# Kernel optimization log

Measured on AMD Instinct MI355X. Metric: run time of the kernel, lower is better.

The kernel has to match this reference:

```python
import jax, jax.numpy as jnp
import numpy as np

EMBED_DIM = 768
NUM_HEADS = 12
HEAD_DIM = EMBED_DIM // NUM_HEADS
B, L = 1, 2048


def setup_inputs() -> dict:
    key = jax.random.key(0)
    ks = jax.random.split(key, 10)
    D = EMBED_DIM
    s = 1.0 / np.sqrt(D)
    x = jax.random.normal(ks[0], (B, L, D), dtype=jnp.float32)
    Wq = jax.random.uniform(ks[1], (D, D), jnp.float32, -s, s)
    bq = jax.random.uniform(ks[2], (D,), jnp.float32, -s, s)
    Wk = jax.random.uniform(ks[3], (D, D), jnp.float32, -s, s)
    bk = jax.random.uniform(ks[4], (D,), jnp.float32, -s, s)
    Wv = jax.random.uniform(ks[5], (D, D), jnp.float32, -s, s)
    bv = jax.random.uniform(ks[6], (D,), jnp.float32, -s, s)
    Wo = jax.random.uniform(ks[7], (D, D), jnp.float32, -s, s)
    bo = jax.random.uniform(ks[8], (D,), jnp.float32, -s, s)
    theta = jnp.zeros((1, NUM_HEADS, 1, 1), dtype=jnp.float32)
    return {"x": x, "Wq": Wq, "bq": bq, "Wk": Wk, "bk": bk,
            "Wv": Wv, "bv": bv, "Wo": Wo, "bo": bo, "theta": theta}


def _heads(t):
    # [B,L,D] -> [B,H,L,d_k]
    b, l, d = t.shape
    return t.reshape(b, l, NUM_HEADS, HEAD_DIM).transpose(0, 2, 1, 3)


def reference(x, Wq, bq, Wk, bk, Wv, bv, Wo, bo, theta):
    b, l, d = x.shape
    d_k = HEAD_DIM
    q = _heads(x @ Wq.T + bq)  # [B,H,L,dk]
    k = _heads(x @ Wk.T + bk)
    v = _heads(x @ Wv.T + bv)
    # squared pairwise L2 distance (== torch.cdist(q,k,p=2)**2), scaled by d_k
    qn = jnp.sum(q * q, axis=-1, keepdims=True)          # [B,H,L,1]
    kn = jnp.sum(k * k, axis=-1, keepdims=True)          # [B,H,L,1]
    qk = jnp.einsum('bhid,bhjd->bhij', q, k)             # [B,H,L,L]
    dist_sq = jnp.maximum(qn + kn.transpose(0, 1, 3, 2) - 2.0 * qk, 0.0) / d_k
    # global max over the full LxL matrix per (B,H)
    dist_max = jnp.max(dist_sq, axis=(-1, -2), keepdims=True)
    dist_norm = dist_sq / (dist_max + 1e-6)
    dsexp = jnp.exp(theta)                               # [1,H,1,1]
    attn_logits = jnp.exp(-dsexp * dist_norm)            # [B,H,L,L]
    attn_weights = jax.nn.softmax(attn_logits, axis=-1)
    context = jnp.einsum('bhij,bhjd->bhid', attn_weights, v)  # [B,H,L,dk]
    context = context.transpose(0, 2, 1, 3).reshape(b, l, d)
    output = context @ Wo.T + bo
    return output, attn_weights.mean(axis=1)
```

## Files before the change

### kernel.cpp

```cpp
#include <hip/hip_runtime.h>
#include <hip/hip_bf16.h>


typedef __bf16 bf16_t;
typedef bf16_t bf16x8 __attribute__((ext_vector_type(8)));
typedef float f32x4 __attribute__((ext_vector_type(4)));

#define L_SEQ 2048
#define DIM 768
#define NH 12
#define DKH 64
#define JSPLIT 4
#define LOG2E 1.44269504f

__device__ __forceinline__ f32x4 mfma16(bf16x8 a, bf16x8 b, f32x4 c_) {
  return __builtin_amdgcn_mfma_f32_16x16x32_bf16(a, b, c_, 0, 0, 0);
}


struct Tile2 { bf16x8 r[2]; };

__device__ __forceinline__ void tile_load(const bf16_t* __restrict__ src, int stride,
                                          Tile2& t_, int tid) {
#pragma unroll
  for (int c = 0; c < 2; ++c) {
    int chunk = tid + c * 256;
    t_.r[c] = *(const bf16x8*)&src[(size_t)(chunk >> 3) * stride + (chunk & 7) * 8];
  }
}

__device__ __forceinline__ void tile_write(bf16_t (*dst)[72], const Tile2& t_, int tid) {
#pragma unroll
  for (int c = 0; c < 2; ++c) {
    int chunk = tid + c * 256;
    *(bf16x8*)&dst[chunk >> 3][(chunk & 7) * 8] = t_.r[c];
  }
}

__device__ __forceinline__ void mfma_nt64(bf16_t (*As)[72], bf16_t (*Bs)[72],
                                          int wid, int lane, f32x4 acc[4]) {
#pragma unroll
  for (int ks = 0; ks < 2; ++ks) {
    bf16x8 a = *(const bf16x8*)&As[wid * 16 + (lane & 15)][ks * 32 + (lane >> 4) * 8];
#pragma unroll
    for (int nt = 0; nt < 4; ++nt) {
      bf16x8 b = *(const bf16x8*)&Bs[nt * 16 + (lane & 15)][ks * 32 + (lane >> 4) * 8];
      acc[nt] = mfma16(a, b, acc[nt]);
    }
  }
}


__global__ void cast_x(const float* __restrict__ in, bf16_t* __restrict__ out, int n4) {
  int i = blockIdx.x * 256 + threadIdx.x;
  if (i >= n4) return;
  float4 v = ((const float4*)in)[i];
  bf16_t* o = out + (size_t)i * 4;
  o[0] = (bf16_t)v.x; o[1] = (bf16_t)v.y; o[2] = (bf16_t)v.z; o[3] = (bf16_t)v.w;
}

__global__ void cast_w4(const float* __restrict__ w0, const float* __restrict__ w1,
                        const float* __restrict__ w2, const float* __restrict__ w3,
                        bf16_t* __restrict__ o0, bf16_t* __restrict__ o1,
                        bf16_t* __restrict__ o2, bf16_t* __restrict__ o3, int n4) {
  int i = blockIdx.x * 256 + threadIdx.x;
  if (i >= n4) return;
  const float* in = blockIdx.y == 0 ? w0 : blockIdx.y == 1 ? w1 : blockIdx.y == 2 ? w2 : w3;
  bf16_t* out = blockIdx.y == 0 ? o0 : blockIdx.y == 1 ? o1 : blockIdx.y == 2 ? o2 : o3;
  float4 v = ((const float4*)in)[i];
  bf16_t* o = out + (size_t)i * 4;
  o[0] = (bf16_t)v.x; o[1] = (bf16_t)v.y; o[2] = (bf16_t)v.z; o[3] = (bf16_t)v.w;
}


__global__ __launch_bounds__(256) void gemm_qkv(const bf16_t* __restrict__ x,
                                                const bf16_t* __restrict__ Bq,
                                                const bf16_t* __restrict__ Bk,
                                                const bf16_t* __restrict__ Bv,
                                                const float* __restrict__ bq,
                                                const float* __restrict__ bk,
                                                const float* __restrict__ bv,
                                                bf16_t* __restrict__ qo,
                                                bf16_t* __restrict__ ko,
                                                bf16_t* __restrict__ vto,
                                                float* __restrict__ qn,
                                                float* __restrict__ kn) {
  __shared__ bf16_t As[2][64][72];
  __shared__ bf16_t Bs[2][64][72];
  const int z = blockIdx.z;
  const bf16_t* B = z == 0 ? Bq : z == 1 ? Bk : Bv;
  const float* bias = z == 0 ? bq : z == 1 ? bk : bv;
  const int tid = threadIdx.x, wid = tid >> 6, lane = tid & 63;
  const int c = lane & 15, hi = lane >> 4;
  const int m0 = blockIdx.y * 64, n0 = blockIdx.x * 64;
  Tile2 at, bt;
  tile_load(x + (size_t)m0 * DIM, DIM, at, tid);
  tile_load(B + (size_t)n0 * DIM, DIM, bt, tid);
  f32x4 acc[4] = {};
  for (int kk = 0; kk < 12; ++kk) {
    tile_write(As[kk & 1], at, tid);
    tile_write(Bs[kk & 1], bt, tid);
    __syncthreads();
    if (kk < 11) {
      tile_load(x + (size_t)m0 * DIM + (kk + 1) * 64, DIM, at, tid);
      tile_load(B + (size_t)n0 * DIM + (kk + 1) * 64, DIM, bt, tid);
    }
    mfma_nt64(As[kk & 1], Bs[kk & 1], wid, lane, acc);
    __syncthreads();
  }
  const int r0 = wid * 16 + hi * 4;
  float ss[4] = {0.f, 0.f, 0.f, 0.f};
#pragma unroll
  for (int nt = 0; nt < 4; ++nt) {
    int cc = n0 + nt * 16 + c;
    float bv_ = bias[cc];
    int h = cc >> 6, d = cc & 63;
#pragma unroll
    for (int r = 0; r < 4; ++r) {
      int mm = m0 + r0 + r;
      float val = acc[nt][r] + bv_;
      if (z == 2) {
        vto[(size_t)cc * L_SEQ + mm] = (bf16_t)val;
      } else {
        bf16_t* out = z == 0 ? qo : ko;
        out[((size_t)h * L_SEQ + mm) * 64 + d] = (bf16_t)val;
        ss[r] = fmaf(val, val, ss[r]);
      }
    }
  }
  if (z < 2) {
#pragma unroll
    for (int s = 1; s < 16; s <<= 1)
#pragma unroll
      for (int r = 0; r < 4; ++r) ss[r] += __shfl_xor(ss[r], s);
    if (c == 0) {
      float* norm = z == 0 ? qn : kn;
      int h = n0 >> 6;
#pragma unroll
      for (int r = 0; r < 4; ++r) norm[h * L_SEQ + m0 + r0 + r] = ss[r];
    }
  }
}

__global__ __launch_bounds__(256) void gemm_out(const bf16_t* __restrict__ A,
                                                const bf16_t* __restrict__ B,
                                                const float* __restrict__ bias,
                                                float* __restrict__ out) {
  __shared__ bf16_t As[2][64][72];
  __shared__ bf16_t Bs[2][64][72];
  const int tid = threadIdx.x, wid = tid >> 6, lane = tid & 63;
  const int c = lane & 15, hi = lane >> 4;
  const int m0 = blockIdx.y * 64, n0 = blockIdx.x * 64;
  Tile2 at, bt;
  tile_load(A + (size_t)m0 * DIM, DIM, at, tid);
  tile_load(B + (size_t)n0 * DIM, DIM, bt, tid);
  f32x4 acc[4] = {};
  for (int kk = 0; kk < 12; ++kk) {
    tile_write(As[kk & 1], at, tid);
    tile_write(Bs[kk & 1], bt, tid);
    __syncthreads();
    if (kk < 11) {
      tile_load(A + (size_t)m0 * DIM + (kk + 1) * 64, DIM, at, tid);
      tile_load(B + (size_t)n0 * DIM + (kk + 1) * 64, DIM, bt, tid);
    }
    mfma_nt64(As[kk & 1], Bs[kk & 1], wid, lane, acc);
    __syncthreads();
  }
  const int r0 = wid * 16 + hi * 4;
#pragma unroll
  for (int nt = 0; nt < 4; ++nt) {
    int cc = n0 + nt * 16 + c;
    float bv = bias[cc];
#pragma unroll
    for (int r = 0; r < 4; ++r)
      out[(size_t)(m0 + r0 + r) * DIM + cc] = acc[nt][r] + bv;
  }
}


__global__ __launch_bounds__(256) void maxdist(const bf16_t* __restrict__ q,
                                               const bf16_t* __restrict__ k,
                                               const float* __restrict__ qn,
                                               const float* __restrict__ kn,
                                               float* __restrict__ blockmax) {
  __shared__ bf16_t Qs[64][72];
  __shared__ bf16_t Ks[64][72];
  __shared__ float wmax[4];
  const int it = blockIdx.x, jc = blockIdx.y, h = blockIdx.z;
  const int i0 = it * 64, jbase = jc * (L_SEQ / JSPLIT);
  const int tid = threadIdx.x, wid = tid >> 6, lane = tid & 63;
  const int c = lane & 15, hi = lane >> 4;
  Tile2 qt, kt;
  tile_load(q + ((size_t)h * L_SEQ + i0) * DKH, DKH, qt, tid);
  tile_write(Qs, qt, tid);
  tile_load(k + ((size_t)h * L_SEQ + jbase) * DKH, DKH, kt, tid);
  const int r0 = wid * 16 + hi * 4;
  float qnr[4];
#pragma unroll
  for (int r = 0; r < 4; ++r) qnr[r] = qn[h * L_SEQ + i0 + r0 + r];
  float m = 0.f;
  const int NT = L_SEQ / 64 / JSPLIT;
  for (int t = 0; t < NT; ++t) {
    tile_write(Ks, kt, tid);
    __syncthreads();
    if (t < NT - 1)
      tile_load(k + ((size_t)h * L_SEQ + jbase + (t + 1) * 64) * DKH, DKH, kt, tid);
    f32x4 acc[4] = {};
    mfma_nt64(Qs, Ks, wid, lane, acc);
#pragma unroll
    for (int nt = 0; nt < 4; ++nt) {
      float knc = kn[h * L_SEQ + jbase + t * 64 + nt * 16 + c];
#pragma unroll
      for (int r = 0; r < 4; ++r)
        m = fmaxf(m, fmaf(-2.f, acc[nt][r], qnr[r] + knc));
    }
    __syncthreads();
  }
#pragma unroll
  for (int s = 1; s < 64; s <<= 1) m = fmaxf(m, __shfl_xor(m, s));
  if (lane == 0) wmax[wid] = m;
  __syncthreads();
  if (tid == 0) {
    float bm = fmaxf(fmaxf(wmax[0], wmax[1]), fmaxf(wmax[2], wmax[3]));
    blockmax[(h * JSPLIT + jc) * (L_SEQ / 64) + it] = fmaxf(bm, 0.f) * (1.f / 64.f);
  }
}

__global__ void reduce_dmax(const float* __restrict__ blockmax, float* __restrict__ dmax) {
  __shared__ float wm[2];
  const int h = blockIdx.x, tid = threadIdx.x, lane = tid & 63, wid = tid >> 6;
  float m = blockmax[h * 128 + tid];
#pragma unroll
  for (int s = 1; s < 64; s <<= 1) m = fmaxf(m, __shfl_xor(m, s));
  if (lane == 0) wm[wid] = m;
  __syncthreads();
  if (tid == 0) dmax[h] = fmaxf(wm[0], wm[1]);
}

__global__ __launch_bounds__(256) void fusedctx_p(const bf16_t* __restrict__ q,
                                                  const bf16_t* __restrict__ k,
                                                  const bf16_t* __restrict__ vt,
                                                  const float* __restrict__ qn,
                                                  const float* __restrict__ kn,
                                                  const float* __restrict__ dmax,
                                                  const float* __restrict__ theta,
                                                  float* __restrict__ denP,
                                                  float* __restrict__ ctxP) {
  __shared__ bf16_t Qs[64][72];
  __shared__ bf16_t Ks[64][72];
  __shared__ bf16_t Vs[64][72];
  __shared__ bf16_t Ws[64][72];
  const int it = blockIdx.x, jc = blockIdx.y, h = blockIdx.z;
  const int i0 = it * 64, jbase = jc * (L_SEQ / 2);
  const int tid = threadIdx.x, wid = tid >> 6, lane = tid & 63;
  const int c = lane & 15, hi = lane >> 4;
  const float sc = __expf(theta[h]) * (1.f / 64.f) / (dmax[h] + 1e-6f);
  const float twosc = 2.f * sc;
  Tile2 qt, kt, vtr;
  tile_load(q + ((size_t)h * L_SEQ + i0) * DKH, DKH, qt, tid);
  tile_write(Qs, qt, tid);
  tile_load(k + ((size_t)h * L_SEQ + jbase) * DKH, DKH, kt, tid);
  tile_load(vt + (size_t)h * DKH * L_SEQ + jbase, L_SEQ, vtr, tid);
  const int r0 = wid * 16 + hi * 4;
  float aq[4];
#pragma unroll
  for (int r = 0; r < 4; ++r) aq[r] = sc * qn[h * L_SEQ + i0 + r0 + r];
  float psum[4] = {0.f, 0.f, 0.f, 0.f};
  f32x4 cacc[4] = {};
  const int NT = L_SEQ / 2 / 64;
  for (int t = 0; t < NT; ++t) {
    tile_write(Ks, kt, tid);
    tile_write(Vs, vtr, tid);
    __syncthreads();
    if (t < NT - 1) {
      tile_load(k + ((size_t)h * L_SEQ + jbase + (t + 1) * 64) * DKH, DKH, kt, tid);
      tile_load(vt + (size_t)h * DKH * L_SEQ + jbase + (t + 1) * 64, L_SEQ, vtr, tid);
    }
    f32x4 acc[4] = {};
    mfma_nt64(Qs, Ks, wid, lane, acc);
#pragma unroll
    for (int nt = 0; nt < 4; ++nt) {
      float bkn = -sc * kn[h * L_SEQ + jbase + t * 64 + nt * 16 + c];
#pragma unroll
      for (int r = 0; r < 4; ++r) {
        float tt = fminf(fmaf(twosc, acc[nt][r], bkn - aq[r]), 0.f);
        float w = __expf(__expf(tt));
        psum[r] += w;
        Ws[r0 + r][nt * 16 + c] = (bf16_t)w;
      }
    }
    __syncthreads();
    mfma_nt64(Vs, Ws, wid, lane, cacc);
    __syncthreads();
  }
#pragma unroll
  for (int s = 1; s < 16; s <<= 1)
#pragma unroll
    for (int r = 0; r < 4; ++r) psum[r] += __shfl_xor(psum[r], s);
  if (c == 0)
#pragma unroll
    for (int r = 0; r < 4; ++r)
      denP[(size_t)(h * 2 + jc) * L_SEQ + i0 + r0 + r] = psum[r];
  float* P = ctxP + ((size_t)(h * 2 + jc) * 32 + it) * 4096;
#pragma unroll
  for (int nt = 0; nt < 4; ++nt)
    *(f32x4*)&P[(nt * 16 + c) * 64 + r0] = cacc[nt];
}

__global__ __launch_bounds__(256) void ctx_combine(const float* __restrict__ denP,
                                                   const float* __restrict__ ctxP,
                                                   float* __restrict__ den,
                                                   bf16_t* __restrict__ ctx) {
  __shared__ float invL[64];
  const int it = blockIdx.x, h = blockIdx.y, tid = threadIdx.x;
  const int i0 = it * 64;
  if (tid < 64) {
    float d0 = denP[(size_t)(h * 2) * L_SEQ + i0 + tid] +
               denP[(size_t)(h * 2 + 1) * L_SEQ + i0 + tid];
    den[h * L_SEQ + i0 + tid] = d0;
    invL[tid] = 1.f / d0;
  }
  __syncthreads();
  const float* P0 = ctxP + ((size_t)(h * 2) * 32 + it) * 4096;
  const float* P1 = ctxP + ((size_t)(h * 2 + 1) * 32 + it) * 4096;
  const int il = tid >> 2, db = (tid & 3) * 16;
  const float inv = invL[il];
  bf16_t* dst = ctx + (size_t)(i0 + il) * DIM + h * 64 + db;
#pragma unroll
  for (int half = 0; half < 2; ++half) {
    bf16x8 o;
#pragma unroll
    for (int e = 0; e < 2; ++e) {
      f32x4 v0 = *(const f32x4*)&P0[il * 64 + db + half * 8 + e * 4];
      f32x4 v1 = *(const f32x4*)&P1[il * 64 + db + half * 8 + e * 4];
#pragma unroll
      for (int j = 0; j < 4; ++j) o[e * 4 + j] = (bf16_t)((v0[j] + v1[j]) * inv);
    }
    *(bf16x8*)&dst[half * 8] = o;
  }
}

__global__ __launch_bounds__(256) void attnmean(const bf16_t* __restrict__ q,
                                                const bf16_t* __restrict__ k,
                                                const float* __restrict__ qn,
                                                const float* __restrict__ kn,
                                                const float* __restrict__ dmax,
                                                const float* __restrict__ theta,
                                                const float* __restrict__ den,
                                                float* __restrict__ out1) {
  __shared__ bf16_t Qs[2][64][72];
  __shared__ bf16_t Ks[2][64][72];
  const int i0 = blockIdx.y * 64, j0 = blockIdx.x * 64;
  const int tid = threadIdx.x, wid = tid >> 6, lane = tid & 63;
  const int c = lane & 15, hi = lane >> 4;
  const int r0 = wid * 16 + hi * 4;
  Tile2 qt, kt;
  tile_load(q + (size_t)i0 * DKH, DKH, qt, tid);
  tile_load(k + (size_t)j0 * DKH, DKH, kt, tid);
  float macc[4][4] = {};
  for (int h = 0; h < NH; ++h) {
    tile_write(Qs[h & 1], qt, tid);
    tile_write(Ks[h & 1], kt, tid);
    __syncthreads();
    if (h < NH - 1) {
      tile_load(q + ((size_t)(h + 1) * L_SEQ + i0) * DKH, DKH, qt, tid);
      tile_load(k + ((size_t)(h + 1) * L_SEQ + j0) * DKH, DKH, kt, tid);
    }
    const float sc = __expf(theta[h]) * (1.f / 64.f) / (dmax[h] + 1e-6f);
    const float twosc = 2.f * sc;
    f32x4 acc[4] = {};
    mfma_nt64(Qs[h & 1], Ks[h & 1], wid, lane, acc);
    float aq[4], invl[4];
#pragma unroll
    for (int r = 0; r < 4; ++r) {
      aq[r] = sc * qn[h * L_SEQ + i0 + r0 + r];
      invl[r] = 1.f / den[h * L_SEQ + i0 + r0 + r];
    }
#pragma unroll
    for (int nt = 0; nt < 4; ++nt) {
      float bkn = -sc * kn[h * L_SEQ + j0 + nt * 16 + c];
#pragma unroll
      for (int r = 0; r < 4; ++r) {
        float tt = fminf(fmaf(twosc, acc[nt][r], bkn - aq[r]), 0.f);
        float w = __expf(__expf(tt));
        macc[nt][r] = fmaf(w, invl[r], macc[nt][r]);
      }
    }
  }
#pragma unroll
  for (int nt = 0; nt < 4; ++nt)
#pragma unroll
    for (int r = 0; r < 4; ++r)
      out1[(size_t)(i0 + r0 + r) * L_SEQ + j0 + nt * 16 + c] =
          macc[nt][r] * (1.f / 12.f);
}


extern "C" void kernel_launch(void* const* d_in, const int* in_sizes, int n_in,
                              void* d_out, int out_size, void* d_ws, size_t ws_size,
                              hipStream_t stream) {
  const float* x = (const float*)d_in[0];
  const float* Wq = (const float*)d_in[1];
  const float* bq = (const float*)d_in[2];
  const float* Wk = (const float*)d_in[3];
  const float* bk = (const float*)d_in[4];
  const float* Wv = (const float*)d_in[5];
  const float* bv = (const float*)d_in[6];
  const float* Wo = (const float*)d_in[7];
  const float* bo = (const float*)d_in[8];
  const float* theta = (const float*)d_in[9];

  bf16_t* x_bf = (bf16_t*)d_ws;
  bf16_t* Wq_bf = x_bf + (size_t)L_SEQ * DIM;
  bf16_t* Wk_bf = Wq_bf + (size_t)DIM * DIM;
  bf16_t* Wv_bf = Wk_bf + (size_t)DIM * DIM;
  bf16_t* Wo_bf = Wv_bf + (size_t)DIM * DIM;
  bf16_t* q_bf = Wo_bf + (size_t)DIM * DIM;
  bf16_t* k_bf = q_bf + (size_t)NH * L_SEQ * DKH;
  bf16_t* vt_bf = k_bf + (size_t)NH * L_SEQ * DKH;
  bf16_t* ctx_bf = vt_bf + (size_t)NH * L_SEQ * DKH;
  float* qn = (float*)(ctx_bf + (size_t)L_SEQ * DIM);
  float* kn = qn + NH * L_SEQ;
  float* den = kn + NH * L_SEQ;
  float* dmax = den + NH * L_SEQ;
  float* blockmax = dmax + 64;
  float* denP = blockmax + 2048;
  float* ctxP = denP + 24 * L_SEQ;

  float* out0 = (float*)d_out;
  float* out1 = out0 + (size_t)L_SEQ * DIM;

  cast_x<<<(L_SEQ * DIM / 4 + 255) / 256, 256, 0, stream>>>(x, x_bf, L_SEQ * DIM / 4);
  cast_w4<<<dim3((DIM * DIM / 4 + 255) / 256, 4), 256, 0, stream>>>(
      Wq, Wk, Wv, Wo, Wq_bf, Wk_bf, Wv_bf, Wo_bf, DIM * DIM / 4);

  gemm_qkv<<<dim3(DIM / 64, L_SEQ / 64, 3), 256, 0, stream>>>(
      x_bf, Wq_bf, Wk_bf, Wv_bf, bq, bk, bv, q_bf, k_bf, vt_bf, qn, kn);

  maxdist<<<dim3(L_SEQ / 64, JSPLIT, NH), 256, 0, stream>>>(q_bf, k_bf, qn, kn, blockmax);
  reduce_dmax<<<NH, 128, 0, stream>>>(blockmax, dmax);

  fusedctx_p<<<dim3(L_SEQ / 64, 2, NH), 256, 0, stream>>>(q_bf, k_bf, vt_bf, qn, kn,
                                                          dmax, theta, denP, ctxP);
  ctx_combine<<<dim3(L_SEQ / 64, NH), 256, 0, stream>>>(denP, ctxP, den, ctx_bf);

  attnmean<<<dim3(L_SEQ / 64, L_SEQ / 64), 256, 0, stream>>>(q_bf, k_bf, qn, kn, dmax,
                                                             theta, den, out1);
  gemm_out<<<dim3(DIM / 64, L_SEQ / 64), 256, 0, stream>>>(ctx_bf, Wo_bf, bo, out0);
}
```

Before: 139.5 us.

## Keep Q fragments in registers, double-buffer K/V, and widen the key split

The maxdist, fusedctx and attnmean kernels now load the Q operand straight from global memory into registers instead of staging it through shared memory. The MFMA is reoriented so that K rows are the A operand, which makes the kn loads vectorised and the out1 stores float4. K and V tiles are double-buffered so one barrier per iteration is dropped, and the P-tile write becomes a vectorised bf16x4 store. fusedctx can also split the key range into 4 chunks instead of 2 when the workspace is large enough, which gives more blocks but adds partial-sum traffic in ctx_combine.

```diff
diff --git a/kernel.cpp b/kernel.cpp
--- a/kernel.cpp
+++ b/kernel.cpp
@@ -4,15 +4,16 @@
 
 typedef __bf16 bf16_t;
 typedef bf16_t bf16x8 __attribute__((ext_vector_type(8)));
+typedef bf16_t bf16x4 __attribute__((ext_vector_type(4)));
 typedef float f32x4 __attribute__((ext_vector_type(4)));
 
 #define L_SEQ 2048
 #define DIM 768
 #define NH 12
 #define DKH 64
-#define JSPLIT 4
-#define LOG2E 1.44269504f
-
+#define MDJ 4
+
+__device__ __forceinline__ bf16x8 ldg8(const bf16_t* p) { return *(const bf16x8*)p; }
 __device__ __forceinline__ f32x4 mfma16(bf16x8 a, bf16x8 b, f32x4 c_) {
   return __builtin_amdgcn_mfma_f32_16x16x32_bf16(a, b, c_, 0, 0, 0);
 }
@@ -177,44 +178,48 @@
   }
 }
 
-
 __global__ __launch_bounds__(256) void maxdist(const bf16_t* __restrict__ q,
                                                const bf16_t* __restrict__ k,
                                                const float* __restrict__ qn,
                                                const float* __restrict__ kn,
                                                float* __restrict__ blockmax) {
-  __shared__ bf16_t Qs[64][72];
-  __shared__ bf16_t Ks[64][72];
+  __shared__ bf16_t Ks[2][64][72];
   __shared__ float wmax[4];
   const int it = blockIdx.x, jc = blockIdx.y, h = blockIdx.z;
-  const int i0 = it * 64, jbase = jc * (L_SEQ / JSPLIT);
+  const int i0 = it * 64, jbase = jc * (L_SEQ / MDJ);
   const int tid = threadIdx.x, wid = tid >> 6, lane = tid & 63;
   const int c = lane & 15, hi = lane >> 4;
-  Tile2 qt, kt;
-  tile_load(q + ((size_t)h * L_SEQ + i0) * DKH, DKH, qt, tid);
-  tile_write(Qs, qt, tid);
+  bf16x8 qb[4][2];
+  float aq[4];
+#pragma unroll
+  for (int nt = 0; nt < 4; ++nt) {
+    const bf16_t* qr = q + ((size_t)h * L_SEQ + i0 + nt * 16 + c) * DKH;
+    qb[nt][0] = ldg8(qr + hi * 8);
+    qb[nt][1] = ldg8(qr + 32 + hi * 8);
+    aq[nt] = qn[h * L_SEQ + i0 + nt * 16 + c];
+  }
+  Tile2 kt;
   tile_load(k + ((size_t)h * L_SEQ + jbase) * DKH, DKH, kt, tid);
-  const int r0 = wid * 16 + hi * 4;
-  float qnr[4];
-#pragma unroll
-  for (int r = 0; r < 4; ++r) qnr[r] = qn[h * L_SEQ + i0 + r0 + r];
   float m = 0.f;
-  const int NT = L_SEQ / 64 / JSPLIT;
+  const int NT = L_SEQ / MDJ / 64;
   for (int t = 0; t < NT; ++t) {
-    tile_write(Ks, kt, tid);
-    __syncthreads();
+    tile_write(Ks[t & 1], kt, tid);
     if (t < NT - 1)
       tile_load(k + ((size_t)h * L_SEQ + jbase + (t + 1) * 64) * DKH, DKH, kt, tid);
+    __syncthreads();
     f32x4 acc[4] = {};
-    mfma_nt64(Qs, Ks, wid, lane, acc);
-#pragma unroll
-    for (int nt = 0; nt < 4; ++nt) {
-      float knc = kn[h * L_SEQ + jbase + t * 64 + nt * 16 + c];
+#pragma unroll
+    for (int ks = 0; ks < 2; ++ks) {
+      bf16x8 a = *(const bf16x8*)&Ks[t & 1][wid * 16 + c][ks * 32 + hi * 8];
+#pragma unroll
+      for (int nt = 0; nt < 4; ++nt) acc[nt] = mfma16(a, qb[nt][ks], acc[nt]);
+    }
+    f32x4 knj = *(const f32x4*)&kn[h * L_SEQ + jbase + t * 64 + wid * 16 + hi * 4];
+#pragma unroll
+    for (int nt = 0; nt < 4; ++nt)
 #pragma unroll
       for (int r = 0; r < 4; ++r)
-        m = fmaxf(m, fmaf(-2.f, acc[nt][r], qnr[r] + knc));
-    }
-    __syncthreads();
+        m = fmaxf(m, fmaf(-2.f, acc[nt][r], aq[nt] + knj[r]));
   }
 #pragma unroll
   for (int s = 1; s < 64; s <<= 1) m = fmaxf(m, __shfl_xor(m, s));
@@ -222,7 +227,7 @@
   __syncthreads();
   if (tid == 0) {
     float bm = fmaxf(fmaxf(wmax[0], wmax[1]), fmaxf(wmax[2], wmax[3]));
-    blockmax[(h * JSPLIT + jc) * (L_SEQ / 64) + it] = fmaxf(bm, 0.f) * (1.f / 64.f);
+    blockmax[(h * MDJ + jc) * (L_SEQ / 64) + it] = fmaxf(bm, 0.f) * (1.f / 64.f);
   }
 }
 
@@ -237,92 +242,114 @@
   if (tid == 0) dmax[h] = fmaxf(wm[0], wm[1]);
 }
 
-__global__ __launch_bounds__(256) void fusedctx_p(const bf16_t* __restrict__ q,
-                                                  const bf16_t* __restrict__ k,
-                                                  const bf16_t* __restrict__ vt,
-                                                  const float* __restrict__ qn,
-                                                  const float* __restrict__ kn,
-                                                  const float* __restrict__ dmax,
-                                                  const float* __restrict__ theta,
-                                                  float* __restrict__ denP,
-                                                  float* __restrict__ ctxP) {
-  __shared__ bf16_t Qs[64][72];
-  __shared__ bf16_t Ks[64][72];
-  __shared__ bf16_t Vs[64][72];
+__global__ __launch_bounds__(256) void fusedctx(const bf16_t* __restrict__ q,
+                                                const bf16_t* __restrict__ k,
+                                                const bf16_t* __restrict__ vt,
+                                                const float* __restrict__ qn,
+                                                const float* __restrict__ kn,
+                                                const float* __restrict__ dmax,
+                                                const float* __restrict__ theta,
+                                                float* __restrict__ denP,
+                                                float* __restrict__ ctxP, int JC) {
+  __shared__ bf16_t Ks[2][64][72];
+  __shared__ bf16_t Vs[2][64][72];
   __shared__ bf16_t Ws[64][72];
+  __shared__ float denW[4][64];
   const int it = blockIdx.x, jc = blockIdx.y, h = blockIdx.z;
-  const int i0 = it * 64, jbase = jc * (L_SEQ / 2);
+  const int i0 = it * 64;
+  const int JLEN = L_SEQ / JC, jbase = jc * JLEN;
   const int tid = threadIdx.x, wid = tid >> 6, lane = tid & 63;
   const int c = lane & 15, hi = lane >> 4;
   const float sc = __expf(theta[h]) * (1.f / 64.f) / (dmax[h] + 1e-6f);
   const float twosc = 2.f * sc;
-  Tile2 qt, kt, vtr;
-  tile_load(q + ((size_t)h * L_SEQ + i0) * DKH, DKH, qt, tid);
-  tile_write(Qs, qt, tid);
+  bf16x8 qb[4][2];
+  float naq[4];
+#pragma unroll
+  for (int nt = 0; nt < 4; ++nt) {
+    const bf16_t* qr = q + ((size_t)h * L_SEQ + i0 + nt * 16 + c) * DKH;
+    qb[nt][0] = ldg8(qr + hi * 8);
+    qb[nt][1] = ldg8(qr + 32 + hi * 8);
+    naq[nt] = -sc * qn[h * L_SEQ + i0 + nt * 16 + c];
+  }
+  Tile2 kt, vtr;
   tile_load(k + ((size_t)h * L_SEQ + jbase) * DKH, DKH, kt, tid);
   tile_load(vt + (size_t)h * DKH * L_SEQ + jbase, L_SEQ, vtr, tid);
-  const int r0 = wid * 16 + hi * 4;
-  float aq[4];
-#pragma unroll
-  for (int r = 0; r < 4; ++r) aq[r] = sc * qn[h * L_SEQ + i0 + r0 + r];
   float psum[4] = {0.f, 0.f, 0.f, 0.f};
   f32x4 cacc[4] = {};
-  const int NT = L_SEQ / 2 / 64;
+  const int NT = JLEN / 64;
   for (int t = 0; t < NT; ++t) {
-    tile_write(Ks, kt, tid);
-    tile_write(Vs, vtr, tid);
-    __syncthreads();
+    tile_write(Ks[t & 1], kt, tid);
+    tile_write(Vs[t & 1], vtr, tid);
     if (t < NT - 1) {
       tile_load(k + ((size_t)h * L_SEQ + jbase + (t + 1) * 64) * DKH, DKH, kt, tid);
       tile_load(vt + (size_t)h * DKH * L_SEQ + jbase + (t + 1) * 64, L_SEQ, vtr, tid);
     }
+    __syncthreads();
     f32x4 acc[4] = {};
-    mfma_nt64(Qs, Ks, wid, lane, acc);
+#pragma unroll
+    for (int ks = 0; ks < 2; ++ks) {
+      bf16x8 a = *(const bf16x8*)&Ks[t & 1][wid * 16 + c][ks * 32 + hi * 8];
+#pragma unroll
+      for (int nt = 0; nt < 4; ++nt) acc[nt] = mfma16(a, qb[nt][ks], acc[nt]);
+    }
+    f32x4 knj = *(const f32x4*)&kn[h * L_SEQ + jbase + t * 64 + wid * 16 + hi * 4];
+    f32x4 sknj = knj * sc;
 #pragma unroll
     for (int nt = 0; nt < 4; ++nt) {
-      float bkn = -sc * kn[h * L_SEQ + jbase + t * 64 + nt * 16 + c];
+      bf16x4 wp;
 #pragma unroll
       for (int r = 0; r < 4; ++r) {
-        float tt = fminf(fmaf(twosc, acc[nt][r], bkn - aq[r]), 0.f);
+        float tt = fminf(fmaf(twosc, acc[nt][r], naq[nt] - sknj[r]), 0.f);
         float w = __expf(__expf(tt));
-        psum[r] += w;
-        Ws[r0 + r][nt * 16 + c] = (bf16_t)w;
+        psum[nt] += w;
+        wp[r] = (bf16_t)w;
       }
-    }
-    __syncthreads();
-    mfma_nt64(Vs, Ws, wid, lane, cacc);
-    __syncthreads();
-  }
-#pragma unroll
-  for (int s = 1; s < 16; s <<= 1)
-#pragma unroll
-    for (int r = 0; r < 4; ++r) psum[r] += __shfl_xor(psum[r], s);
-  if (c == 0)
-#pragma unroll
-    for (int r = 0; r < 4; ++r)
-      denP[(size_t)(h * 2 + jc) * L_SEQ + i0 + r0 + r] = psum[r];
-  float* P = ctxP + ((size_t)(h * 2 + jc) * 32 + it) * 4096;
+      *(bf16x4*)&Ws[nt * 16 + c][wid * 16 + hi * 4] = wp;
+    }
+    __syncthreads();
+#pragma unroll
+    for (int ks = 0; ks < 2; ++ks) {
+      bf16x8 a = *(const bf16x8*)&Vs[t & 1][wid * 16 + c][ks * 32 + hi * 8];
+#pragma unroll
+      for (int nt = 0; nt < 4; ++nt) {
+        bf16x8 b = *(const bf16x8*)&Ws[nt * 16 + c][ks * 32 + hi * 8];
+        cacc[nt] = mfma16(a, b, cacc[nt]);
+      }
+    }
+  }
+#pragma unroll
+  for (int nt = 0; nt < 4; ++nt) {
+    psum[nt] += __shfl_xor(psum[nt], 16);
+    psum[nt] += __shfl_xor(psum[nt], 32);
+  }
+  if (lane < 16)
+#pragma unroll
+    for (int nt = 0; nt < 4; ++nt) denW[wid][nt * 16 + lane] = psum[nt];
+  __syncthreads();
+  if (tid < 64)
+    denP[(size_t)(h * JC + jc) * L_SEQ + i0 + tid] =
+        denW[0][tid] + denW[1][tid] + denW[2][tid] + denW[3][tid];
+  float* P = ctxP + ((size_t)(h * JC + jc) * 32 + it) * 4096;
 #pragma unroll
   for (int nt = 0; nt < 4; ++nt)
-    *(f32x4*)&P[(nt * 16 + c) * 64 + r0] = cacc[nt];
+    *(f32x4*)&P[(nt * 16 + c) * 64 + wid * 16 + hi * 4] = cacc[nt];
 }
 
 __global__ __launch_bounds__(256) void ctx_combine(const float* __restrict__ denP,
                                                    const float* __restrict__ ctxP,
                                                    float* __restrict__ den,
-                                                   bf16_t* __restrict__ ctx) {
+                                                   bf16_t* __restrict__ ctx, int JC) {
   __shared__ float invL[64];
   const int it = blockIdx.x, h = blockIdx.y, tid = threadIdx.x;
   const int i0 = it * 64;
   if (tid < 64) {
-    float d0 = denP[(size_t)(h * 2) * L_SEQ + i0 + tid] +
-               denP[(size_t)(h * 2 + 1) * L_SEQ + i0 + tid];
+    float d0 = 0.f;
+    for (int jc = 0; jc < JC; ++jc)
+      d0 += denP[(size_t)(h * JC + jc) * L_SEQ + i0 + tid];
     den[h * L_SEQ + i0 + tid] = d0;
     invL[tid] = 1.f / d0;
   }
   __syncthreads();
-  const float* P0 = ctxP + ((size_t)(h * 2) * 32 + it) * 4096;
-  const float* P1 = ctxP + ((size_t)(h * 2 + 1) * 32 + it) * 4096;
   const int il = tid >> 2, db = (tid & 3) * 16;
   const float inv = invL[il];
   bf16_t* dst = ctx + (size_t)(i0 + il) * DIM + h * 64 + db;
@@ -331,10 +358,12 @@
     bf16x8 o;
 #pragma unroll
     for (int e = 0; e < 2; ++e) {
-      f32x4 v0 = *(const f32x4*)&P0[il * 64 + db + half * 8 + e * 4];
-      f32x4 v1 = *(const f32x4*)&P1[il * 64 + db + half * 8 + e * 4];
-#pragma unroll
-      for (int j = 0; j < 4; ++j) o[e * 4 + j] = (bf16_t)((v0[j] + v1[j]) * inv);
+      f32x4 v = {0.f, 0.f, 0.f, 0.f};
+      for (int jc = 0; jc < JC; ++jc)
+        v += *(const f32x4*)&ctxP[((size_t)(h * JC + jc) * 32 + it) * 4096 +
+                                  il * 64 + db + half * 8 + e * 4];
+#pragma unroll
+      for (int j = 0; j < 4; ++j) o[e * 4 + j] = (bf16_t)(v[j] * inv);
     }
     *(bf16x8*)&dst[half * 8] = o;
   }
@@ -348,51 +377,48 @@
                                                 const float* __restrict__ theta,
                                                 const float* __restrict__ den,
                                                 float* __restrict__ out1) {
-  __shared__ bf16_t Qs[2][64][72];
-  __shared__ bf16_t Ks[2][64][72];
-  const int i0 = blockIdx.y * 64, j0 = blockIdx.x * 64;
+  const int j0 = blockIdx.x * 64, i0 = blockIdx.y * 64;
   const int tid = threadIdx.x, wid = tid >> 6, lane = tid & 63;
   const int c = lane & 15, hi = lane >> 4;
-  const int r0 = wid * 16 + hi * 4;
-  Tile2 qt, kt;
-  tile_load(q + (size_t)i0 * DKH, DKH, qt, tid);
-  tile_load(k + (size_t)j0 * DKH, DKH, kt, tid);
-  float macc[4][4] = {};
+  f32x4 macc[4] = {};
   for (int h = 0; h < NH; ++h) {
-    tile_write(Qs[h & 1], qt, tid);
-    tile_write(Ks[h & 1], kt, tid);
-    __syncthreads();
-    if (h < NH - 1) {
-      tile_load(q + ((size_t)(h + 1) * L_SEQ + i0) * DKH, DKH, qt, tid);
-      tile_load(k + ((size_t)(h + 1) * L_SEQ + j0) * DKH, DKH, kt, tid);
-    }
     const float sc = __expf(theta[h]) * (1.f / 64.f) / (dmax[h] + 1e-6f);
     const float twosc = 2.f * sc;
+    const bf16_t* kr = k + ((size_t)h * L_SEQ + j0 + wid * 16 + c) * DKH;
+    bf16x8 ka0 = ldg8(kr + hi * 8);
+    bf16x8 ka1 = ldg8(kr + 32 + hi * 8);
+    bf16x8 qb[4][2];
+#pragma unroll
+    for (int nt = 0; nt < 4; ++nt) {
+      const bf16_t* qr = q + ((size_t)h * L_SEQ + i0 + nt * 16 + c) * DKH;
+      qb[nt][0] = ldg8(qr + hi * 8);
+      qb[nt][1] = ldg8(qr + 32 + hi * 8);
+    }
     f32x4 acc[4] = {};
-    mfma_nt64(Qs[h & 1], Ks[h & 1], wid, lane, acc);
-    float aq[4], invl[4];
-#pragma unroll
-    for (int r = 0; r < 4; ++r) {
-      aq[r] = sc * qn[h * L_SEQ + i0 + r0 + r];
-      invl[r] = 1.f / den[h * L_SEQ + i0 + r0 + r];
-    }
 #pragma unroll
     for (int nt = 0; nt < 4; ++nt) {
-      float bkn = -sc * kn[h * L_SEQ + j0 + nt * 16 + c];
+      acc[nt] = mfma16(ka0, qb[nt][0], acc[nt]);
+      acc[nt] = mfma16(ka1, qb[nt][1], acc[nt]);
+    }
+    f32x4 knj = *(const f32x4*)&kn[h * L_SEQ + j0 + wid * 16 + hi * 4];
+    f32x4 sknj = knj * sc;
+#pragma unroll
+    for (int nt = 0; nt < 4; ++nt) {
+      float naq = -sc * qn[h * L_SEQ + i0 + nt * 16 + c];
+      float inv = 1.f / den[h * L_SEQ + i0 + nt * 16 + c];
 #pragma unroll
       for (int r = 0; r < 4; ++r) {
-        float tt = fminf(fmaf(twosc, acc[nt][r], bkn - aq[r]), 0.f);
+        float tt = fminf(fmaf(twosc, acc[nt][r], naq - sknj[r]), 0.f);
         float w = __expf(__expf(tt));
-        macc[nt][r] = fmaf(w, invl[r], macc[nt][r]);
+        macc[nt][r] = fmaf(w, inv, macc[nt][r]);
       }
     }
   }
 #pragma unroll
-  for (int nt = 0; nt < 4; ++nt)
-#pragma unroll
-    for (int r = 0; r < 4; ++r)
-      out1[(size_t)(i0 + r0 + r) * L_SEQ + j0 + nt * 16 + c] =
-          macc[nt][r] * (1.f / 12.f);
+  for (int nt = 0; nt < 4; ++nt) {
+    f32x4 o = macc[nt] * (1.f / 12.f);
+    *(f32x4*)&out1[(size_t)(i0 + nt * 16 + c) * L_SEQ + j0 + wid * 16 + hi * 4] = o;
+  }
 }
 
 
@@ -425,7 +451,10 @@
   float* dmax = den + NH * L_SEQ;
   float* blockmax = dmax + 64;
   float* denP = blockmax + 2048;
-  float* ctxP = denP + 24 * L_SEQ;
+  float* ctxP = denP + 4 * NH * L_SEQ;
+
+  size_t fixed_bytes = (size_t)((char*)ctxP - (char*)d_ws);
+  int JC = (fixed_bytes + (size_t)4 * NH * 32 * 4096 * 4 <= ws_size) ? 4 : 2;
 
   float* out0 = (float*)d_out;
   float* out1 = out0 + (size_t)L_SEQ * DIM;
@@ -437,12 +466,12 @@
   gemm_qkv<<<dim3(DIM / 64, L_SEQ / 64, 3), 256, 0, stream>>>(
       x_bf, Wq_bf, Wk_bf, Wv_bf, bq, bk, bv, q_bf, k_bf, vt_bf, qn, kn);
 
-  maxdist<<<dim3(L_SEQ / 64, JSPLIT, NH), 256, 0, stream>>>(q_bf, k_bf, qn, kn, blockmax);
+  maxdist<<<dim3(L_SEQ / 64, MDJ, NH), 256, 0, stream>>>(q_bf, k_bf, qn, kn, blockmax);
   reduce_dmax<<<NH, 128, 0, stream>>>(blockmax, dmax);
 
-  fusedctx_p<<<dim3(L_SEQ / 64, 2, NH), 256, 0, stream>>>(q_bf, k_bf, vt_bf, qn, kn,
-                                                          dmax, theta, denP, ctxP);
-  ctx_combine<<<dim3(L_SEQ / 64, NH), 256, 0, stream>>>(denP, ctxP, den, ctx_bf);
+  fusedctx<<<dim3(L_SEQ / 64, JC, NH), 256, 0, stream>>>(q_bf, k_bf, vt_bf, qn, kn,
+                                                         dmax, theta, denP, ctxP, JC);
+  ctx_combine<<<dim3(L_SEQ / 64, NH), 256, 0, stream>>>(denP, ctxP, den, ctx_bf, JC);
 
   attnmean<<<dim3(L_SEQ / 64, L_SEQ / 64), 256, 0, stream>>>(q_bf, k_bf, qn, kn, dmax,
                                                              theta, den, out1);
```

Result: slower. 175.0 us (+25.4%).
